# Kernel tuning notes

Hardware: AMD Instinct MI355X
Metric: run time of the kernel (lower is better)

Reference implementation:

```python
import jax, jax.numpy as jnp
import numpy as np
from jax import lax

B, H, W, C = 2, 256, 256, 192
HEADS = 6
WS = 8                      # window size
PW = WS // 2                # permuted window size (kv downsampled 2x2)
HIDDEN = 4 * C
HEAD_DIM = C // HEADS
SCALE = HEAD_DIM ** -0.5
N_WIN = WS * WS             # 64 query tokens per window
N_KV = PW * PW              # 16 kv tokens per window


def _aligned_index(pw0, pw1):
    ch = np.arange(pw0)
    cw = np.arange(pw1)
    coords = np.stack(np.meshgrid(ch, cw, indexing='ij'))          # (2, pw0, pw1)
    cf = coords.reshape(2, -1)
    rel = (cf[:, :, None] - cf[:, None, :]).transpose(1, 2, 0).astype(np.int64)
    rel[:, :, 0] += pw0 - 1
    rel[:, :, 1] += pw1 - 1
    rel[:, :, 0] *= 2 * pw1 - 1
    idx = rel.sum(-1)                                              # (N_KV, N_KV)
    n4 = pw0 * pw1
    idx = idx.reshape(pw0, pw1, 1, 1, n4)
    idx = np.tile(idx, (1, 1, 2, 2, 1)).transpose(0, 2, 1, 3, 4).reshape(4 * n4, n4)
    return jnp.asarray(idx)

IDX = _aligned_index(PW, PW)   # (N_WIN, N_KV)


def layernorm(x, g, b):
    mu = x.mean(-1, keepdims=True)
    var = ((x - mu) ** 2).mean(-1, keepdims=True)
    return (x - mu) * lax.rsqrt(var + 1e-5) * g + b


def window_partition(x):
    # (B, H, W, C) -> (B*nW, WS, WS, C)
    x = x.reshape(B, H // WS, WS, W // WS, WS, C)
    return x.transpose(0, 1, 3, 2, 4, 5).reshape(-1, WS, WS, C)


def window_reverse(w):
    # (B*nW, WS, WS, C) -> (B, H, W, C)
    x = w.reshape(B, H // WS, W // WS, WS, WS, C)
    return x.transpose(0, 1, 3, 2, 4, 5).reshape(B, H, W, C)


def setup_inputs() -> dict:
    key = jax.random.key(0)
    ks = jax.random.split(key, 10)
    rn = lambda k, shp, s=0.02: jax.random.normal(k, shp, jnp.float32) * s
    return {
        'x': jax.random.normal(ks[0], (B, H * W, C), jnp.float32),
        'g1': jnp.ones((C,), jnp.float32), 'be1': jnp.zeros((C,), jnp.float32),
        'wq': rn(ks[1], (C, C)), 'bq': jnp.zeros((C,), jnp.float32),
        'wkv': rn(ks[2], (C, C // 2)), 'bkv': jnp.zeros((C // 2,), jnp.float32),
        'bias_table': rn(ks[3], ((2 * PW - 1) * (2 * PW - 1), HEADS)),
        'wproj': rn(ks[4], (C, C)), 'bproj': jnp.zeros((C,), jnp.float32),
        'g2': jnp.ones((C,), jnp.float32), 'be2': jnp.zeros((C,), jnp.float32),
        'w1f': rn(ks[5], (C, HIDDEN)), 'b1f': jnp.zeros((HIDDEN,), jnp.float32),
        'dwk': rn(ks[6], (HIDDEN, 1, 5, 5)), 'dwb': jnp.zeros((HIDDEN,), jnp.float32),
        'w2f': rn(ks[7], (HIDDEN, C)), 'b2f': jnp.zeros((C,), jnp.float32),
    }


def reference(x, g1, be1, wq, bq, wkv, bkv, bias_table, wproj, bproj,
              g2, be2, w1f, b1f, dwk, dwb, w2f, b2f):
    shortcut = x
    xn = layernorm(x, g1, be1).reshape(B, H, W, C)
    xw = window_partition(xn).reshape(-1, N_WIN, C)        # (b_, 64, C)
    b_ = xw.shape[0]
    # PSA: kv downsampled 2x2 spatially, 2x2 block folded into channels
    kv = (xw @ wkv + bkv).reshape(b_, PW, 2, PW, 2, 2, C // 4)
    kv = kv.transpose(0, 1, 3, 5, 2, 4, 6).reshape(b_, N_KV, 2, HEADS, HEAD_DIM)
    kv = kv.transpose(2, 0, 3, 1, 4)                       # (2, b_, h, N_KV, d)
    k, v = kv[0], kv[1]
    q = (xw @ wq + bq).reshape(b_, N_WIN, HEADS, HEAD_DIM).transpose(0, 2, 1, 3) * SCALE
    attn = jnp.einsum('bhqd,bhkd->bhqk', q, k)             # (b_, h, 64, 16)
    bias = bias_table[IDX.reshape(-1)].reshape(N_WIN, N_KV, HEADS).transpose(2, 0, 1)
    attn = jax.nn.softmax(attn + bias[None], axis=-1)
    aw = jnp.einsum('bhqk,bhkd->bhqd', attn, v).transpose(0, 2, 1, 3).reshape(b_, N_WIN, C)
    aw = aw @ wproj + bproj
    x = shortcut + window_reverse(aw.reshape(-1, WS, WS, C)).reshape(B, H * W, C)
    # ConvFFN with depthwise-conv residual branch
    xn2 = layernorm(x, g2, be2)
    h1 = jax.nn.gelu(xn2 @ w1f + b1f, approximate=False)   # (B, HW, HIDDEN)
    img = h1.transpose(0, 2, 1).reshape(B, HIDDEN, H, W)
    conv = lax.conv_general_dilated(img, dwk, (1, 1), ((2, 2), (2, 2)),
                                    feature_group_count=HIDDEN,
                                    dimension_numbers=('NCHW', 'OIHW', 'NCHW'))
    conv = jax.nn.gelu(conv + dwb[None, :, None, None], approximate=False)
    h = h1 + conv.reshape(B, HIDDEN, H * W).transpose(0, 2, 1)
    return x + (h @ w2f + b2f)
```

## Files before the change

### kernel.cpp

```cpp
#include <hip/hip_runtime.h>
#include <hip/hip_bf16.h>
#include <math.h>

#define NTOK  131072
#define NTOKH 65536
#define CD    192
#define HID   768

typedef short bf16x8 __attribute__((ext_vector_type(8)));
typedef float f32x4  __attribute__((ext_vector_type(4)));

__device__ __forceinline__ float bf2f(unsigned short v) {
    union { unsigned int u; float f; } c; c.u = ((unsigned int)v) << 16; return c.f;
}
__device__ __forceinline__ unsigned short f2bf(float f) {
    __hip_bfloat16 h = __float2bfloat16(f);
    return *reinterpret_cast<unsigned short*>(&h);
}
__device__ __forceinline__ float gelu_f(float x) {
    return 0.5f * x * (1.0f + erff(x * 0.7071067811865476f));
}

__global__ __launch_bounds__(256) void ln_kernel(const float* __restrict__ x,
                                                 const float* __restrict__ g,
                                                 const float* __restrict__ b,
                                                 unsigned short* __restrict__ out) {
    int tok  = blockIdx.x * 4 + (threadIdx.x >> 6);
    int lane = threadIdx.x & 63;
    const float* xp = x + (size_t)tok * CD;
    float v0 = xp[lane], v1 = xp[lane + 64], v2 = xp[lane + 128];
    float s  = v0 + v1 + v2;
    float s2 = v0 * v0 + v1 * v1 + v2 * v2;
    #pragma unroll
    for (int off = 32; off > 0; off >>= 1) {
        s  += __shfl_xor(s,  off, 64);
        s2 += __shfl_xor(s2, off, 64);
    }
    float mu  = s * (1.0f / 192.0f);
    float var = s2 * (1.0f / 192.0f) - mu * mu;
    float rs  = rsqrtf(var + 1e-5f);
    unsigned short* op = out + (size_t)tok * CD;
    op[lane]       = f2bf((v0 - mu) * rs * g[lane]       + b[lane]);
    op[lane + 64]  = f2bf((v1 - mu) * rs * g[lane + 64]  + b[lane + 64]);
    op[lane + 128] = f2bf((v2 - mu) * rs * g[lane + 128] + b[lane + 128]);
}

__global__ __launch_bounds__(256) void wconv_kernel(
    const float* __restrict__ wq, const float* __restrict__ wkv,
    const float* __restrict__ wproj, const float* __restrict__ w1f,
    const float* __restrict__ w2f,
    unsigned short* __restrict__ qkvT, unsigned short* __restrict__ projT,
    unsigned short* __restrict__ w1T, unsigned short* __restrict__ w2T)
{
    int i = blockIdx.x * 256 + threadIdx.x;
    if (i < 288 * 192) {
        int n = i / 192, k = i - n * 192;
        float v = (n < 192) ? wq[(size_t)k * 192 + n] : wkv[(size_t)k * 96 + (n - 192)];
        qkvT[n * 192 + k] = f2bf(v);
    }
    if (i < 192 * 192) {
        int n = i / 192, k = i - n * 192;
        projT[n * 192 + k] = f2bf(wproj[(size_t)k * 192 + n]);
    }
    {
        int n = i / 192, k = i - n * 192;
        w1T[n * 192 + k] = f2bf(w1f[(size_t)k * 768 + n]);
    }
    {
        int n = i / 768, k = i - n * 768;
        w2T[n * 768 + k] = f2bf(w2f[(size_t)k * 192 + n]);
    }
}

template<int MODE>
__global__ __launch_bounds__(256) void mgemm_kernel(
    const unsigned short* __restrict__ A,
    const unsigned short* __restrict__ WT,
    const float* __restrict__ b0, const float* __restrict__ b1,
    const float* __restrict__ addsrc,
    void* O0, unsigned short* __restrict__ O1,
    int K, int Nreal)
{
    constexpr int BM = 128, BN = 64, BK = 64;
    constexpr int LDA = BK + 8;
    __shared__ unsigned short As[BM * LDA];
    __shared__ unsigned short Bs[BN * LDA];
    const int tid  = threadIdx.x;
    const int wave = tid >> 6, lane = tid & 63;
    const int quad = lane >> 4, l16 = lane & 15;
    const int wm = (wave >> 1) * 64, wn = (wave & 1) * 32;
    const int m0 = blockIdx.y * BM, n0 = blockIdx.x * BN;

    f32x4 acc[4][2];
    #pragma unroll
    for (int mi = 0; mi < 4; mi++)
        #pragma unroll
        for (int ni = 0; ni < 2; ni++) acc[mi][ni] = (f32x4){0.f, 0.f, 0.f, 0.f};

    const int ar  = tid >> 1;
    const int ak  = (tid & 1) * 32;
    const int br  = tid >> 2;
    const int bk  = (tid & 3) * 16;

    for (int k0 = 0; k0 < K; k0 += BK) {
        #pragma unroll
        for (int c = 0; c < 4; c++)
            *(uint4*)&As[ar * LDA + ak + c * 8] =
                *(const uint4*)(A + (size_t)(m0 + ar) * K + k0 + ak + c * 8);
        #pragma unroll
        for (int c = 0; c < 2; c++) {
            uint4 wv = make_uint4(0u, 0u, 0u, 0u);
            if (n0 + br < Nreal)
                wv = *(const uint4*)(WT + (size_t)(n0 + br) * K + k0 + bk + c * 8);
            *(uint4*)&Bs[br * LDA + bk + c * 8] = wv;
        }
        __syncthreads();

        #pragma unroll
        for (int kk = 0; kk < 2; kk++) {
            bf16x8 bf[2];
            #pragma unroll
            for (int ni = 0; ni < 2; ni++)
                bf[ni] = *(const bf16x8*)&Bs[(wn + ni * 16 + l16) * LDA + kk * 32 + quad * 8];
            #pragma unroll
            for (int mi = 0; mi < 4; mi++) {
                bf16x8 af = *(const bf16x8*)&As[(wm + mi * 16 + l16) * LDA + kk * 32 + quad * 8];
                acc[mi][0] = __builtin_amdgcn_mfma_f32_16x16x32_bf16(af, bf[0], acc[mi][0], 0, 0, 0);
                acc[mi][1] = __builtin_amdgcn_mfma_f32_16x16x32_bf16(af, bf[1], acc[mi][1], 0, 0, 0);
            }
        }
        __syncthreads();
    }

    #pragma unroll
    for (int mi = 0; mi < 4; mi++) {
        int row0 = m0 + wm + mi * 16 + quad * 4;
        #pragma unroll
        for (int ni = 0; ni < 2; ni++) {
            int col = n0 + wn + ni * 16 + l16;
            #pragma unroll
            for (int r = 0; r < 4; r++) {
                size_t m = (size_t)(row0 + r);
                float v = acc[mi][ni][r];
                if (MODE == 0) {
                    if (col < 192)
                        ((unsigned short*)O0)[m * 192 + col] =
                            f2bf((v + b0[col]) * 0.17677669529663687f);
                    else if (col < 288)
                        O1[m * 96 + (col - 192)] = f2bf(v + b1[col - 192]);
                } else if (MODE == 1) {
                    ((float*)O0)[m * 192 + col] = v + b0[col] + addsrc[m * 192 + col];
                } else if (MODE == 2) {
                    ((unsigned short*)O0)[m * 768 + col] = f2bf(gelu_f(v + b0[col]));
                } else {
                    float* op = (float*)O0;
                    op[m * 192 + col] = op[m * 192 + col] + v + b0[col];
                }
            }
        }
    }
}

__global__ __launch_bounds__(384) void attn_kernel(
    const unsigned short* __restrict__ q, const unsigned short* __restrict__ kvp,
    const float* __restrict__ bt, unsigned short* __restrict__ aw)
{
    __shared__ float ks[6][16][32];
    __shared__ float vs[6][16][32];
    const int w = blockIdx.x;
    const int b = w >> 10, rem = w & 1023, wh = rem >> 5, wc = rem & 31;
    const int tid = threadIdx.x;
    const size_t base = (size_t)b * 65536;

    for (int e = tid; e < 16 * 192; e += 384) {
        int kk = e / 192, f = e - kk * 192;
        int d1 = kk >> 2, d3 = kk & 3;
        int d2 = f / 96;  int r = f - d2 * 96;
        int d4 = r / 48;  int c4 = r - d4 * 48;
        int i = 2 * d1 + d2, j = 2 * d3 + d4;
        size_t g = base + (size_t)(wh * 8 + i) * 256 + (wc * 8 + j);
        int h = f >> 5, d = f & 31;
        ks[h][kk][d] = bf2f(kvp[g * 96 + c4]);
        vs[h][kk][d] = bf2f(kvp[g * 96 + 48 + c4]);
    }
    __syncthreads();

    const int t = tid & 63, h = tid >> 6;
    const int i = t >> 3, j = t & 7;
    const int iq2 = i >> 1, jq2 = j >> 1;
    const size_t g = base + (size_t)(wh * 8 + i) * 256 + (wc * 8 + j);

    float qr[32];
    const ushort4* qp = (const ushort4*)(q + g * 192 + h * 32);
    #pragma unroll
    for (int d4i = 0; d4i < 8; d4i++) {
        ushort4 u = qp[d4i];
        qr[d4i * 4 + 0] = bf2f(u.x); qr[d4i * 4 + 1] = bf2f(u.y);
        qr[d4i * 4 + 2] = bf2f(u.z); qr[d4i * 4 + 3] = bf2f(u.w);
    }

    float lg[16]; float mx = -1e30f;
    #pragma unroll
    for (int kk = 0; kk < 16; kk++) {
        int kh = kk >> 2, kw = kk & 3;
        float s = bt[((iq2 - kh + 3) * 7 + (jq2 - kw + 3)) * 6 + h];
        #pragma unroll
        for (int d = 0; d < 32; d++) s = fmaf(qr[d], ks[h][kk][d], s);
        lg[kk] = s; mx = fmaxf(mx, s);
    }
    float den = 0.f;
    #pragma unroll
    for (int kk = 0; kk < 16; kk++) { lg[kk] = expf(lg[kk] - mx); den += lg[kk]; }
    float inv = 1.0f / den;

    float oacc[32];
    #pragma unroll
    for (int d = 0; d < 32; d++) oacc[d] = 0.f;
    #pragma unroll
    for (int kk = 0; kk < 16; kk++) {
        float p = lg[kk] * inv;
        #pragma unroll
        for (int d = 0; d < 32; d++) oacc[d] = fmaf(p, vs[h][kk][d], oacc[d]);
    }
    unsigned short* op = aw + g * 192 + h * 32;
    #pragma unroll
    for (int d = 0; d < 32; d++) op[d] = f2bf(oacc[d]);
}

__global__ __launch_bounds__(256) void dwconv_kernel(
    const unsigned short* __restrict__ h1,
    const float* __restrict__ dwk, const float* __restrict__ dwb,
    unsigned short* __restrict__ hout)
{
    __shared__ float tile[12][12][64];
    int bx = blockIdx.x;
    int chb = bx % 12; int t = bx / 12;
    int tw = t % 32; int th = t / 32;
    const int tid = threadIdx.x;
    const int chbase = chb * 64;
    const int ch = tid & 63;
    const int cp = tid >> 6;
    const int c0 = cp * 2;

    float w[25];
    #pragma unroll
    for (int tap = 0; tap < 25; tap++)
        w[tap] = dwk[(size_t)(chbase + ch) * 25 + tap];
    const float bias = dwb[chbase + ch];

    const int lane4 = tid & 15;
    const int pg = tid >> 4;
    for (int p = pg; p < 144; p += 16) {
        int pr = p / 12, pc = p - pr * 12;
        int r = th * 8 - 2 + pr, c = tw * 8 - 2 + pc;
        float f0 = 0.f, f1 = 0.f, f2 = 0.f, f3 = 0.f;
        if (r >= 0 && r < 256 && c >= 0 && c < 256) {
            const unsigned short* sp = h1 + (((size_t)r * 256 + c) * HID + chbase + lane4 * 4);
            ushort4 u = *(const ushort4*)sp;
            f0 = bf2f(u.x); f1 = bf2f(u.y); f2 = bf2f(u.z); f3 = bf2f(u.w);
        }
        tile[pr][pc][lane4 * 4 + 0] = f0;
        tile[pr][pc][lane4 * 4 + 1] = f1;
        tile[pr][pc][lane4 * 4 + 2] = f2;
        tile[pr][pc][lane4 * 4 + 3] = f3;
    }
    __syncthreads();

    float win[5][6];
    #pragma unroll
    for (int rr = 0; rr < 4; rr++)
        #pragma unroll
        for (int cc = 0; cc < 6; cc++)
            win[rr][cc] = tile[rr][c0 + cc][ch];

    #pragma unroll
    for (int r0 = 0; r0 < 8; r0++) {
        #pragma unroll
        for (int cc = 0; cc < 6; cc++)
            win[(r0 + 4) % 5][cc] = tile[r0 + 4][c0 + cc][ch];
        float s0 = bias, s1 = bias;
        #pragma unroll
        for (int kr = 0; kr < 5; kr++) {
            int ri = (r0 + kr) % 5;
            #pragma unroll
            for (int kc = 0; kc < 5; kc++) {
                float wt = w[kr * 5 + kc];
                s0 = fmaf(win[ri][kc],     wt, s0);
                s1 = fmaf(win[ri][kc + 1], wt, s1);
            }
        }
        float v0 = win[(r0 + 2) % 5][2] + gelu_f(s0);
        float v1 = win[(r0 + 2) % 5][3] + gelu_f(s1);
        size_t tok = (size_t)(th * 8 + r0) * 256 + tw * 8 + c0;
        hout[tok * HID + chbase + ch]         = f2bf(v0);
        hout[(tok + 1) * HID + chbase + ch]   = f2bf(v1);
    }
}

extern "C" void kernel_launch(void* const* d_in, const int* in_sizes, int n_in,
                              void* d_out, int out_size, void* d_ws, size_t ws_size,
                              hipStream_t stream) {
    const float* x    = (const float*)d_in[0];
    const float* g1   = (const float*)d_in[1];
    const float* be1  = (const float*)d_in[2];
    const float* wq   = (const float*)d_in[3];
    const float* bq   = (const float*)d_in[4];
    const float* wkv  = (const float*)d_in[5];
    const float* bkv  = (const float*)d_in[6];
    const float* btab = (const float*)d_in[7];
    const float* wproj= (const float*)d_in[8];
    const float* bproj= (const float*)d_in[9];
    const float* g2   = (const float*)d_in[10];
    const float* be2  = (const float*)d_in[11];
    const float* w1f  = (const float*)d_in[12];
    const float* b1f  = (const float*)d_in[13];
    const float* dwk  = (const float*)d_in[14];
    const float* dwb  = (const float*)d_in[15];
    const float* w2f  = (const float*)d_in[16];
    const float* b2f  = (const float*)d_in[17];
    float* out = (float*)d_out;

    char* ws = (char*)d_ws;
    unsigned short* xnb  = (unsigned short*)(ws);
    unsigned short* qb   = (unsigned short*)(ws + 50331648);
    unsigned short* kvb  = (unsigned short*)(ws + 100663296);
    unsigned short* h1b  = (unsigned short*)(ws + 125829120);
    unsigned short* hhb  = (unsigned short*)(ws + 226492416);
    unsigned short* qkvT = (unsigned short*)(ws + 327155712);
    unsigned short* projT= (unsigned short*)(ws + 327266304);
    unsigned short* w1T  = (unsigned short*)(ws + 327340032);
    unsigned short* w2T  = (unsigned short*)(ws + 327634944);

    wconv_kernel<<<576, 256, 0, stream>>>(wq, wkv, wproj, w1f, w2f,
                                          qkvT, projT, w1T, w2T);
    ln_kernel<<<NTOK / 4, 256, 0, stream>>>(x, g1, be1, xnb);
    mgemm_kernel<0><<<dim3(5, NTOK / 128), 256, 0, stream>>>(
        xnb, qkvT, bq, bkv, nullptr, qb, kvb, 192, 288);
    attn_kernel<<<2048, 384, 0, stream>>>(qb, kvb, btab, xnb);
    mgemm_kernel<1><<<dim3(3, NTOK / 128), 256, 0, stream>>>(
        xnb, projT, bproj, nullptr, x, out, nullptr, 192, 192);
    ln_kernel<<<NTOK / 4, 256, 0, stream>>>(out, g2, be2, qb);
    for (int half = 0; half < 2; half++) {
        const unsigned short* xn2h = qb + (size_t)half * NTOKH * CD;
        float* outh = out + (size_t)half * NTOKH * CD;
        mgemm_kernel<2><<<dim3(12, NTOKH / 128), 256, 0, stream>>>(
            xn2h, w1T, b1f, nullptr, nullptr, h1b, nullptr, 192, 768);
        dwconv_kernel<<<12 * 32 * 32, 256, 0, stream>>>(h1b, dwk, dwb, hhb);
        mgemm_kernel<3><<<dim3(3, NTOKH / 128), 256, 0, stream>>>(
            hhb, w2T, b2f, nullptr, nullptr, outh, nullptr, 768, 192);
    }
}
```

Baseline: 906.0 us.

## Widen GEMM N-tile to 96 with direct-to-LDS loads and XOR swizzle

```diff
diff --git a/kernel.cpp b/kernel.cpp
--- a/kernel.cpp
+++ b/kernel.cpp
@@ -19,6 +19,13 @@
 }
 __device__ __forceinline__ float gelu_f(float x) {
     return 0.5f * x * (1.0f + erff(x * 0.7071067811865476f));
+}
+
+__device__ __forceinline__ void gld16(const unsigned short* g, unsigned short* l) {
+    __builtin_amdgcn_global_load_lds(
+        (const __attribute__((address_space(1))) void*)(unsigned long long)(g),
+        (__attribute__((address_space(3))) void*)(unsigned int)(unsigned long long)(l),
+        16, 0, 0);
 }
 
 __global__ __launch_bounds__(256) void ln_kernel(const float* __restrict__ x,
@@ -81,52 +88,53 @@
     void* O0, unsigned short* __restrict__ O1,
     int K, int Nreal)
 {
-    constexpr int BM = 128, BN = 64, BK = 64;
-    constexpr int LDA = BK + 8;
-    __shared__ unsigned short As[BM * LDA];
-    __shared__ unsigned short Bs[BN * LDA];
+    constexpr int BM = 128, BN = 96, BK = 64;
+    __shared__ unsigned short As[BM * BK];
+    __shared__ unsigned short Bs[BN * BK];
     const int tid  = threadIdx.x;
     const int wave = tid >> 6, lane = tid & 63;
     const int quad = lane >> 4, l16 = lane & 15;
-    const int wm = (wave >> 1) * 64, wn = (wave & 1) * 32;
+    const int wm = (wave >> 1) * 64, wn = (wave & 1) * 48;
     const int m0 = blockIdx.y * BM, n0 = blockIdx.x * BN;
 
-    f32x4 acc[4][2];
+    f32x4 acc[4][3];
     #pragma unroll
     for (int mi = 0; mi < 4; mi++)
         #pragma unroll
-        for (int ni = 0; ni < 2; ni++) acc[mi][ni] = (f32x4){0.f, 0.f, 0.f, 0.f};
-
-    const int ar  = tid >> 1;
-    const int ak  = (tid & 1) * 32;
-    const int br  = tid >> 2;
-    const int bk  = (tid & 3) * 16;
+        for (int ni = 0; ni < 3; ni++) acc[mi][ni] = (f32x4){0.f, 0.f, 0.f, 0.f};
+
+    const int r8 = lane >> 3;
+    const int sw = ((lane & 7) ^ r8) << 3;
+    const unsigned short* aSrc = A  + (size_t)(m0 + wave * 32 + r8) * K + sw;
+    const unsigned short* bSrc = WT + (size_t)(n0 + wave * 24 + r8) * K + sw;
+    unsigned short* aDst = &As[(wave * 32) * BK];
+    unsigned short* bDst = &Bs[(wave * 24) * BK];
 
     for (int k0 = 0; k0 < K; k0 += BK) {
         #pragma unroll
-        for (int c = 0; c < 4; c++)
-            *(uint4*)&As[ar * LDA + ak + c * 8] =
-                *(const uint4*)(A + (size_t)(m0 + ar) * K + k0 + ak + c * 8);
-        #pragma unroll
-        for (int c = 0; c < 2; c++) {
-            uint4 wv = make_uint4(0u, 0u, 0u, 0u);
-            if (n0 + br < Nreal)
-                wv = *(const uint4*)(WT + (size_t)(n0 + br) * K + k0 + bk + c * 8);
-            *(uint4*)&Bs[br * LDA + bk + c * 8] = wv;
-        }
+        for (int i = 0; i < 4; i++)
+            gld16(aSrc + k0 + i * 8 * K, aDst + i * 8 * BK);
+        #pragma unroll
+        for (int i = 0; i < 3; i++)
+            gld16(bSrc + k0 + i * 8 * K, bDst + i * 8 * BK);
         __syncthreads();
 
         #pragma unroll
         for (int kk = 0; kk < 2; kk++) {
-            bf16x8 bf[2];
+            const int cb = kk * 64 + quad * 16;
+            bf16x8 bfr[3];
             #pragma unroll
-            for (int ni = 0; ni < 2; ni++)
-                bf[ni] = *(const bf16x8*)&Bs[(wn + ni * 16 + l16) * LDA + kk * 32 + quad * 8];
+            for (int ni = 0; ni < 3; ni++) {
+                int br = wn + ni * 16 + l16;
+                bfr[ni] = *(const bf16x8*)&Bs[br * BK + ((cb ^ ((br & 7) << 4)) >> 1)];
+            }
             #pragma unroll
             for (int mi = 0; mi < 4; mi++) {
-                bf16x8 af = *(const bf16x8*)&As[(wm + mi * 16 + l16) * LDA + kk * 32 + quad * 8];
-                acc[mi][0] = __builtin_amdgcn_mfma_f32_16x16x32_bf16(af, bf[0], acc[mi][0], 0, 0, 0);
-                acc[mi][1] = __builtin_amdgcn_mfma_f32_16x16x32_bf16(af, bf[1], acc[mi][1], 0, 0, 0);
+                int ar = wm + mi * 16 + l16;
+                bf16x8 af = *(const bf16x8*)&As[ar * BK + ((cb ^ ((ar & 7) << 4)) >> 1)];
+                acc[mi][0] = __builtin_amdgcn_mfma_f32_16x16x32_bf16(af, bfr[0], acc[mi][0], 0, 0, 0);
+                acc[mi][1] = __builtin_amdgcn_mfma_f32_16x16x32_bf16(af, bfr[1], acc[mi][1], 0, 0, 0);
+                acc[mi][2] = __builtin_amdgcn_mfma_f32_16x16x32_bf16(af, bfr[2], acc[mi][2], 0, 0, 0);
             }
         }
         __syncthreads();
@@ -136,7 +144,7 @@
     for (int mi = 0; mi < 4; mi++) {
         int row0 = m0 + wm + mi * 16 + quad * 4;
         #pragma unroll
-        for (int ni = 0; ni < 2; ni++) {
+        for (int ni = 0; ni < 3; ni++) {
             int col = n0 + wn + ni * 16 + l16;
             #pragma unroll
             for (int r = 0; r < 4; r++) {
@@ -146,7 +154,7 @@
                     if (col < 192)
                         ((unsigned short*)O0)[m * 192 + col] =
                             f2bf((v + b0[col]) * 0.17677669529663687f);
-                    else if (col < 288)
+                    else
                         O1[m * 96 + (col - 192)] = f2bf(v + b1[col - 192]);
                 } else if (MODE == 1) {
                     ((float*)O0)[m * 192 + col] = v + b0[col] + addsrc[m * 192 + col];
@@ -334,19 +342,19 @@
     wconv_kernel<<<576, 256, 0, stream>>>(wq, wkv, wproj, w1f, w2f,
                                           qkvT, projT, w1T, w2T);
     ln_kernel<<<NTOK / 4, 256, 0, stream>>>(x, g1, be1, xnb);
-    mgemm_kernel<0><<<dim3(5, NTOK / 128), 256, 0, stream>>>(
+    mgemm_kernel<0><<<dim3(3, NTOK / 128), 256, 0, stream>>>(
         xnb, qkvT, bq, bkv, nullptr, qb, kvb, 192, 288);
     attn_kernel<<<2048, 384, 0, stream>>>(qb, kvb, btab, xnb);
-    mgemm_kernel<1><<<dim3(3, NTOK / 128), 256, 0, stream>>>(
+    mgemm_kernel<1><<<dim3(2, NTOK / 128), 256, 0, stream>>>(
         xnb, projT, bproj, nullptr, x, out, nullptr, 192, 192);
     ln_kernel<<<NTOK / 4, 256, 0, stream>>>(out, g2, be2, qb);
     for (int half = 0; half < 2; half++) {
         const unsigned short* xn2h = qb + (size_t)half * NTOKH * CD;
         float* outh = out + (size_t)half * NTOKH * CD;
-        mgemm_kernel<2><<<dim3(12, NTOKH / 128), 256, 0, stream>>>(
+        mgemm_kernel<2><<<dim3(8, NTOKH / 128), 256, 0, stream>>>(
             xn2h, w1T, b1f, nullptr, nullptr, h1b, nullptr, 192, 768);
         dwconv_kernel<<<12 * 32 * 32, 256, 0, stream>>>(h1b, dwk, dwb, hhb);
-        mgemm_kernel<3><<<dim3(3, NTOKH / 128), 256, 0, stream>>>(
+        mgemm_kernel<3><<<dim3(2, NTOKH / 128), 256, 0, stream>>>(
             hhb, w2T, b2f, nullptr, nullptr, outh, nullptr, 768, 192);
     }
 }
```

After: 804.3 us. 11.2% less time.
